# Kernel tuning notes

Hardware: AMD Instinct MI355X
Metric: run time of the kernel (lower is better)

The kernel has to match this reference:

```python
import jax, jax.numpy as jnp
import numpy as np
from jax import lax

EPS = 1e-5

def rmsnorm(x, w, eps=EPS):
    x = jnp.clip(x, -100.0, 100.0)
    var = jnp.clip(jnp.mean(x * x, axis=-1, keepdims=True), eps, None)
    x = jnp.clip(x * lax.rsqrt(var + eps), -10.0, 10.0)
    return w * x

def activation_quant(x):
    x = jnp.clip(x, -50.0, 50.0)
    max_val = jnp.clip(jnp.max(jnp.abs(x), axis=-1, keepdims=True), 0.0001, None)
    scale = 127.0 / max_val
    return jnp.clip(jnp.round(x * scale), -128, 127) / scale

def weight_quant(w):
    scale = jnp.clip(jnp.mean(jnp.abs(w)), 1e-8, None)
    return jnp.sign(w - jnp.mean(w)) * scale

def bitlinear(x, w, norm_w):
    # x: [T, in], w: [out, in], norm_w: [in]
    xn = rmsnorm(x, norm_w)
    xq = xn + lax.stop_gradient(activation_quant(xn) - xn)
    wq = w + lax.stop_gradient(weight_quant(w) - w)
    return jnp.einsum('ti,oi->to', xq, wq)

def expert_fwd(x, wg, wu, wd, n_g, n_u, n_d):
    gate = jnp.clip(bitlinear(x, wg, n_g), -20.0, 20.0)
    up = bitlinear(x, wu, n_u)
    hidden = jnp.clip(jax.nn.silu(gate) * up, -1000.0, 1000.0)
    return bitlinear(hidden, wd, n_d)

def setup_inputs() -> dict:
    key = jax.random.key(0)
    B, S, H, I, E = 4, 2048, 768, 2048, 8
    ks = jax.random.split(key, 12)
    std_h = 0.02 / np.sqrt(H)
    std_i = 0.02 / np.sqrt(I)
    return {
        'hidden_states': jax.random.normal(ks[0], (B, S, H), jnp.float32),
        'router_w': 0.01 * jax.random.normal(ks[1], (E, H), jnp.float32),
        'router_b': jnp.zeros((E,), jnp.float32),
        'Wg': std_h * jax.random.normal(ks[2], (E, I, H), jnp.float32),
        'Wu': std_h * jax.random.normal(ks[3], (E, I, H), jnp.float32),
        'Wd': std_i * jax.random.normal(ks[4], (E, H, I), jnp.float32),
        'ng': jnp.ones((E, H), jnp.float32),
        'nu': jnp.ones((E, H), jnp.float32),
        'nd': jnp.ones((E, I), jnp.float32),
        'sWg': std_h * jax.random.normal(ks[5], (I, H), jnp.float32),
        'sWu': std_h * jax.random.normal(ks[6], (I, H), jnp.float32),
        'sWd': std_i * jax.random.normal(ks[7], (H, I), jnp.float32),
        'sng': jnp.ones((H,), jnp.float32),
        'snu': jnp.ones((H,), jnp.float32),
        'snd': jnp.ones((I,), jnp.float32),
    }

def reference(hidden_states, router_w, router_b, Wg, Wu, Wd, ng, nu, nd, sWg, sWu, sWd, sng, snu, snd):
    B, S, H = hidden_states.shape
    E = router_w.shape[0]
    K = 2  # num_experts_per_tok
    x = hidden_states.reshape(-1, H)  # [T, H]
    router_logits = jnp.einsum('th,eh->te', x, router_w) + router_b  # [T, E]
    routing_weights = jax.nn.softmax(router_logits, axis=-1)
    top_w, top_idx = lax.top_k(routing_weights, K)  # [T, K]
    top_w = top_w / (jnp.sum(top_w, axis=-1, keepdims=True) + 1e-8)
    out = jnp.zeros_like(x)
    for e in range(E):
        w_e = jnp.sum(jnp.where(top_idx == e, top_w, 0.0), axis=-1)  # [T]
        y_e = expert_fwd(x, Wg[e], Wu[e], Wd[e], ng[e], nu[e], nd[e])
        out = out + y_e * w_e[:, None]
    out = out + expert_fwd(x, sWg, sWu, sWd, sng, snu, snd)
    out = jnp.clip(out, -10000.0, 10000.0)
    return out.reshape(B, S, H), router_logits
```

## Files before the change

### kernel.cpp

```cpp
#include <hip/hip_runtime.h>
#include <hip/hip_bf16.h>
#include <math.h>

#define TOK 8192
#define HD 768
#define ID 2048
#define NE 8
#define MSIZE (2048*768)
#define BM 128
#define BK 64
#define R_SHARED 8192
#define R_MAX 25600

typedef int v4i __attribute__((ext_vector_type(4)));
typedef __attribute__((address_space(1))) void gas_void;
typedef __attribute__((address_space(3))) void las_void;

__device__ __forceinline__ void g2lds16(const void* g, void* l) {
  __builtin_amdgcn_global_load_lds((gas_void*)g, (las_void*)l, 16, 0, 0);
}

__device__ __forceinline__ float clipf(float v, float lo, float hi) {
  return fminf(fmaxf(v, lo), hi);
}

__device__ __forceinline__ const float* matsel(int mat, const float* Wg, const float* Wu,
                                               const float* Wd, const float* sWg,
                                               const float* sWu, const float* sWd) {
  if (mat < 8)  return Wg + (size_t)mat * MSIZE;
  if (mat < 16) return Wu + (size_t)(mat - 8) * MSIZE;
  if (mat < 24) return Wd + (size_t)(mat - 16) * MSIZE;
  if (mat == 24) return sWg;
  if (mat == 25) return sWu;
  return sWd;
}

__global__ __launch_bounds__(256)
void k_wstats(const float* __restrict__ Wg, const float* __restrict__ Wu,
              const float* __restrict__ Wd, const float* __restrict__ sWg,
              const float* __restrict__ sWu, const float* __restrict__ sWd,
              double* __restrict__ stats) {
  int mat = blockIdx.y;
  const float* p = matsel(mat, Wg, Wu, Wd, sWg, sWu, sWd);
  int tid = threadIdx.x;
  double s = 0.0, sa = 0.0;
  for (size_t i = (size_t)blockIdx.x * 256 + tid; i < (size_t)MSIZE;
       i += (size_t)gridDim.x * 256) {
    double v = (double)p[i];
    s += v; sa += fabs(v);
  }
  __shared__ double rs[256], ra[256];
  rs[tid] = s; ra[tid] = sa; __syncthreads();
  for (int st = 128; st > 0; st >>= 1) {
    if (tid < st) { rs[tid] += rs[tid + st]; ra[tid] += ra[tid + st]; }
    __syncthreads();
  }
  if (tid == 0) {
    atomicAdd(&stats[mat * 2 + 0], rs[0]);
    atomicAdd(&stats[mat * 2 + 1], ra[0]);
  }
}

__global__ void k_wfinal(const double* __restrict__ stats, double* __restrict__ wmean,
                         float* __restrict__ wscale) {
  int m = threadIdx.x;
  if (m < 27) {
    wmean[m] = stats[m * 2] / (double)MSIZE;
    double sc = stats[m * 2 + 1] / (double)MSIZE;
    wscale[m] = (float)fmax(sc, 1e-8);
  }
}

__global__ __launch_bounds__(256)
void k_wquant(const float* __restrict__ Wg, const float* __restrict__ Wu,
              const float* __restrict__ Wd, const float* __restrict__ sWg,
              const float* __restrict__ sWu, const float* __restrict__ sWd,
              const double* __restrict__ wmean, signed char* __restrict__ tw) {
  int mat = blockIdx.y;
  const float* p = matsel(mat, Wg, Wu, Wd, sWg, sWu, sWd);
  const float4* p4 = (const float4*)p;
  int* t4 = (int*)(tw + (size_t)mat * MSIZE);
  double mu = wmean[mat];
  for (int i = blockIdx.x * 256 + threadIdx.x; i < MSIZE / 4; i += gridDim.x * 256) {
    float4 v = p4[i];
    int b0 = ((double)v.x > mu) ? 1 : (((double)v.x < mu) ? -1 : 0);
    int b1 = ((double)v.y > mu) ? 1 : (((double)v.y < mu) ? -1 : 0);
    int b2 = ((double)v.z > mu) ? 1 : (((double)v.z < mu) ? -1 : 0);
    int b3 = ((double)v.w > mu) ? 1 : (((double)v.w < mu) ? -1 : 0);
    t4[i] = (b0 & 255) | ((b1 & 255) << 8) | ((b2 & 255) << 16) | ((b3 & 255) << 24);
  }
}

__global__ __launch_bounds__(256)
void k_router(const float* __restrict__ x, const float* __restrict__ rw,
              const float* __restrict__ rb, float* __restrict__ logits,
              int* __restrict__ top_idx, float* __restrict__ top_w) {
  int wv = threadIdx.x >> 6, ln = threadIdx.x & 63;
  int t = blockIdx.x * 4 + wv;
  const float4* xr = (const float4*)(x + (size_t)t * HD);
  const float4* rw4 = (const float4*)rw;
  float acc[NE] = {};
#pragma unroll
  for (int i = 0; i < 3; ++i) {
    float4 xv = xr[ln + i * 64];
#pragma unroll
    for (int e = 0; e < NE; ++e) {
      float4 w4 = rw4[e * 192 + ln + i * 64];
      acc[e] += xv.x * w4.x + xv.y * w4.y + xv.z * w4.z + xv.w * w4.w;
    }
  }
#pragma unroll
  for (int e = 0; e < NE; ++e) {
    float v = acc[e];
#pragma unroll
    for (int o = 32; o > 0; o >>= 1) v += __shfl_down(v, o, 64);
    acc[e] = v;
  }
  if (ln == 0) {
    float lg[NE], m = -1e30f;
#pragma unroll
    for (int e = 0; e < NE; ++e) {
      lg[e] = acc[e] + rb[e];
      logits[(size_t)t * NE + e] = lg[e];
      m = fmaxf(m, lg[e]);
    }
    float p[NE], s = 0.f;
#pragma unroll
    for (int e = 0; e < NE; ++e) { p[e] = expf(lg[e] - m); s += p[e]; }
    float inv = 1.f / s;
#pragma unroll
    for (int e = 0; e < NE; ++e) p[e] *= inv;
    int e1 = 0; float b1 = p[0];
    for (int e = 1; e < NE; ++e) if (p[e] > b1) { b1 = p[e]; e1 = e; }
    int e2 = -1; float b2 = -1.f;
    for (int e = 0; e < NE; ++e) if (e != e1 && p[e] > b2) { b2 = p[e]; e2 = e; }
    float sw = b1 + b2 + 1e-8f;
    top_idx[t * 2 + 0] = e1; top_idx[t * 2 + 1] = e2;
    top_w[t * 2 + 0] = b1 / sw; top_w[t * 2 + 1] = b2 / sw;
  }
}

__global__ __launch_bounds__(1024)
void k_hist(const int* __restrict__ top_idx, int* __restrict__ counts) {
  __shared__ int h[NE];
  if (threadIdx.x < NE) h[threadIdx.x] = 0;
  __syncthreads();
  for (int i = threadIdx.x; i < TOK * 2; i += 1024) atomicAdd(&h[top_idx[i]], 1);
  __syncthreads();
  if (threadIdx.x < NE) counts[threadIdx.x] = h[threadIdx.x];
}

__global__ void k_initrows(int* __restrict__ rows_token, float* __restrict__ rows_w,
                           int* __restrict__ rows_expert) {
  int r = blockIdx.x * blockDim.x + threadIdx.x;
  if (r >= R_MAX) return;
  if (r < R_SHARED) { rows_token[r] = r; rows_w[r] = 1.f; rows_expert[r] = NE; }
  else { rows_token[r] = -1; rows_w[r] = 0.f; rows_expert[r] = 0; }
}

__global__ void k_offsets(const int* __restrict__ counts, int* __restrict__ offs,
                          int* __restrict__ fill) {
  if (threadIdx.x == 0) {
    int off = R_SHARED;
    for (int e = 0; e < NE; ++e) {
      offs[e] = off;
      off += ((counts[e] + BM - 1) / BM) * BM;
    }
    offs[NE] = off;
  }
  if (threadIdx.x < NE) fill[threadIdx.x] = 0;
}

__global__ __launch_bounds__(256)
void k_scatter(const int* __restrict__ top_idx, const float* __restrict__ top_w,
               const int* __restrict__ offs, int* __restrict__ fill,
               int* __restrict__ rows_token, float* __restrict__ rows_w,
               int* __restrict__ rows_expert, int* __restrict__ inv_row) {
  int t = blockIdx.x * 256 + threadIdx.x;
  int ln = threadIdx.x & 63;
  unsigned long long lt = (ln == 63) ? 0x7fffffffffffffffull
                                     : ((1ull << ln) - 1);
#pragma unroll
  for (int k = 0; k < 2; ++k) {
    int e = top_idx[t * 2 + k];
    unsigned long long peers = 0;
#pragma unroll
    for (int ee = 0; ee < NE; ++ee) {
      unsigned long long m = __ballot(e == ee);
      if (e == ee) peers = m;
    }
    int lead = __ffsll(peers) - 1;
    int rank = __popcll(peers & lt);
    int base = 0;
    if (ln == lead) base = atomicAdd(&fill[e], __popcll(peers));
    base = __shfl(base, lead, 64);
    int r = offs[e] + base + rank;
    rows_token[r] = t;
    rows_w[r] = top_w[t * 2 + k];
    rows_expert[r] = e;
    inv_row[t * 2 + k] = r;
  }
}

__global__ __launch_bounds__(256)
void k_actquant(const float* __restrict__ x, const int* __restrict__ rows_token,
                const int* __restrict__ rows_expert, const float* __restrict__ ng,
                const float* __restrict__ nu, const float* __restrict__ sng,
                const float* __restrict__ snu, signed char* __restrict__ xqg,
                signed char* __restrict__ xqu, float* __restrict__ invg,
                float* __restrict__ invu) {
  int r = blockIdx.x, tid = threadIdx.x;
  int tok = rows_token[r];
  if (tok < 0) {
    for (int i = tid; i < HD; i += 256) {
      xqg[(size_t)r * HD + i] = 0; xqu[(size_t)r * HD + i] = 0;
    }
    if (tid == 0) { invg[r] = 0.f; invu[r] = 0.f; }
    return;
  }
  int e = rows_expert[r];
  const float* wg = (e < NE) ? ng + (size_t)e * HD : sng;
  const float* wu = (e < NE) ? nu + (size_t)e * HD : snu;
  __shared__ float red[256];
  float xv[3]; float ss = 0.f;
#pragma unroll
  for (int i = 0; i < 3; ++i) {
    float v = x[(size_t)tok * HD + tid + i * 256];
    v = clipf(v, -100.f, 100.f);
    xv[i] = v; ss += v * v;
  }
  red[tid] = ss; __syncthreads();
  for (int st = 128; st > 0; st >>= 1) { if (tid < st) red[tid] += red[tid + st]; __syncthreads(); }
  float var = fmaxf(red[0] / (float)HD, 1e-5f);
  __syncthreads();
  float rinv = rsqrtf(var + 1e-5f);
  float xn[3]; float amax = 0.f;
#pragma unroll
  for (int i = 0; i < 3; ++i) {
    float t = clipf(xv[i] * rinv, -10.f, 10.f) * wg[tid + i * 256];
    t = clipf(t, -50.f, 50.f);
    xn[i] = t; amax = fmaxf(amax, fabsf(t));
  }
  red[tid] = amax; __syncthreads();
  for (int st = 128; st > 0; st >>= 1) { if (tid < st) red[tid] = fmaxf(red[tid], red[tid + st]); __syncthreads(); }
  float mx = fmaxf(red[0], 1e-4f);
  __syncthreads();
  float sc = 127.f / mx;
#pragma unroll
  for (int i = 0; i < 3; ++i)
    xqg[(size_t)r * HD + tid + i * 256] = (signed char)(int)clipf(rintf(xn[i] * sc), -128.f, 127.f);
  if (tid == 0) invg[r] = 1.f / sc;
  amax = 0.f;
#pragma unroll
  for (int i = 0; i < 3; ++i) {
    float t = clipf(xv[i] * rinv, -10.f, 10.f) * wu[tid + i * 256];
    t = clipf(t, -50.f, 50.f);
    xn[i] = t; amax = fmaxf(amax, fabsf(t));
  }
  red[tid] = amax; __syncthreads();
  for (int st = 128; st > 0; st >>= 1) { if (tid < st) red[tid] = fmaxf(red[tid], red[tid + st]); __syncthreads(); }
  mx = fmaxf(red[0], 1e-4f);
  __syncthreads();
  sc = 127.f / mx;
#pragma unroll
  for (int i = 0; i < 3; ++i)
    xqu[(size_t)r * HD + tid + i * 256] = (signed char)(int)clipf(rintf(xn[i] * sc), -128.f, 127.f);
  if (tid == 0) invu[r] = 1.f / sc;
}

__global__ __launch_bounds__(256, 2)
void k_gemm_gu(const signed char* __restrict__ xqg, const signed char* __restrict__ xqu,
               const signed char* __restrict__ tw, const float* __restrict__ wscale,
               const float* __restrict__ invg, const float* __restrict__ invu,
               const int* __restrict__ rows_expert, const int* __restrict__ offs,
               __hip_bfloat16* __restrict__ hidden) {
  int n0 = blockIdx.x * BM;
  int row0 = blockIdx.y * BM;
  if (row0 >= offs[NE]) return;
  int e = rows_expert[row0];
  int mg = (e < NE) ? e : 24;
  int mu = (e < NE) ? e + 8 : 25;
  const signed char* wgp = tw + (size_t)mg * MSIZE;
  const signed char* wup = tw + (size_t)mu * MSIZE;
  __shared__ __align__(16) signed char Ag[2 * BM * BK];
  __shared__ __align__(16) signed char Au[2 * BM * BK];
  __shared__ __align__(16) signed char Bg[2 * BM * BK];
  __shared__ __align__(16) signed char Bu[2 * BM * BK];
  __shared__ float sg[BM], su[BM];
  int tid = threadIdx.x, wv = tid >> 6, ln = tid & 63;
  if (tid < BM) { sg[tid] = invg[row0 + tid]; su[tid] = invu[row0 + tid]; }
  v4i accg[4][4] = {};
  v4i accu[4][4] = {};
  int lr = ln >> 2;
  int swz = (((ln & 3) ^ ((lr >> 1) & 3)) << 4);
  const signed char* pag[2]; const signed char* pau[2];
  const signed char* pbg[2]; const signed char* pbu[2];
#pragma unroll
  for (int j = 0; j < 2; ++j) {
    int row = (wv * 2 + j) * 16 + lr;
    pag[j] = xqg + (size_t)(row0 + row) * HD + swz;
    pau[j] = xqu + (size_t)(row0 + row) * HD + swz;
    pbg[j] = wgp + (size_t)(n0 + row) * HD + swz;
    pbu[j] = wup + (size_t)(n0 + row) * HD + swz;
  }
  int wm = (wv & 1) * 64, wn = (wv >> 1) * 64;
  int fm = ln & 15;
  int slot16 = (((ln >> 4) ^ ((fm >> 1) & 3)) << 4);
  int offA[4], offB[4];
#pragma unroll
  for (int i = 0; i < 4; ++i) offA[i] = (wm + i * 16 + fm) * BK + slot16;
#pragma unroll
  for (int j = 0; j < 4; ++j) offB[j] = (wn + j * 16 + fm) * BK + slot16;

  auto stage = [&](int buf) {
#pragma unroll
    for (int j = 0; j < 2; ++j) {
      int co = buf * 8192 + (wv * 2 + j) * 1024;
      g2lds16(pag[j], &Ag[co]);
      g2lds16(pau[j], &Au[co]);
      g2lds16(pbg[j], &Bg[co]);
      g2lds16(pbu[j], &Bu[co]);
      pag[j] += BK; pau[j] += BK; pbg[j] += BK; pbu[j] += BK;
    }
  };
  auto compute = [&](int buf) {
    int lb = buf * 8192;
    v4i ag[4], au[4];
#pragma unroll
    for (int i = 0; i < 4; ++i) {
      ag[i] = *(const v4i*)&Ag[lb + offA[i]];
      au[i] = *(const v4i*)&Au[lb + offA[i]];
    }
#pragma unroll
    for (int j = 0; j < 4; ++j) {
      v4i bg = *(const v4i*)&Bg[lb + offB[j]];
      v4i bu = *(const v4i*)&Bu[lb + offB[j]];
#pragma unroll
      for (int i = 0; i < 4; ++i) {
        accg[i][j] = __builtin_amdgcn_mfma_i32_16x16x64_i8(ag[i], bg, accg[i][j], 0, 0, 0);
        accu[i][j] = __builtin_amdgcn_mfma_i32_16x16x64_i8(au[i], bu, accu[i][j], 0, 0, 0);
      }
    }
  };

  const int NIT = HD / BK;
  stage(0);
#pragma unroll 1
  for (int it = 0; it < NIT; it += 2) {
    __syncthreads();
    if (it + 1 < NIT) stage(1);
    compute(0);
    __syncthreads();
    if (it + 2 < NIT) stage(0);
    compute(1);
  }

  float gs = wscale[mg], us = wscale[mu];
  int dq = (ln >> 4) * 4, dn = ln & 15;
  for (int i = 0; i < 4; ++i) {
#pragma unroll
    for (int rg = 0; rg < 4; ++rg) {
      int lrow = wm + i * 16 + dq + rg;
      int grow = row0 + lrow;
      float ig = gs * sg[lrow];
      float iu = us * su[lrow];
#pragma unroll
      for (int j = 0; j < 4; ++j) {
        int gcol = n0 + wn + j * 16 + dn;
        float g = (float)accg[i][j][rg] * ig;
        g = clipf(g, -20.f, 20.f);
        float sil = g / (1.f + expf(-g));
        float u = (float)accu[i][j][rg] * iu;
        float h = clipf(sil * u, -1000.f, 1000.f);
        hidden[(size_t)grow * ID + gcol] = __float2bfloat16(h);
      }
    }
  }
}

__global__ __launch_bounds__(256)
void k_hquant(const __hip_bfloat16* __restrict__ hidden, const int* __restrict__ rows_token,
              const int* __restrict__ rows_expert, const float* __restrict__ nd,
              const float* __restrict__ snd, signed char* __restrict__ hq,
              float* __restrict__ invh) {
  int r = blockIdx.x, tid = threadIdx.x;
  int tok = rows_token[r];
  if (tok < 0) {
    for (int i = tid; i < ID; i += 256) hq[(size_t)r * ID + i] = 0;
    if (tid == 0) invh[r] = 0.f;
    return;
  }
  int e = rows_expert[r];
  const float* wn = (e < NE) ? nd + (size_t)e * ID : snd;
  __shared__ float red[256];
  float xv[8]; float ss = 0.f;
#pragma unroll
  for (int i = 0; i < 8; ++i) {
    float v = __bfloat162float(hidden[(size_t)r * ID + tid + i * 256]);
    v = clipf(v, -100.f, 100.f);
    xv[i] = v; ss += v * v;
  }
  red[tid] = ss; __syncthreads();
  for (int st = 128; st > 0; st >>= 1) { if (tid < st) red[tid] += red[tid + st]; __syncthreads(); }
  float var = fmaxf(red[0] / (float)ID, 1e-5f);
  __syncthreads();
  float rinv = rsqrtf(var + 1e-5f);
  float xn[8]; float amax = 0.f;
#pragma unroll
  for (int i = 0; i < 8; ++i) {
    float t = clipf(xv[i] * rinv, -10.f, 10.f) * wn[tid + i * 256];
    t = clipf(t, -50.f, 50.f);
    xn[i] = t; amax = fmaxf(amax, fabsf(t));
  }
  red[tid] = amax; __syncthreads();
  for (int st = 128; st > 0; st >>= 1) { if (tid < st) red[tid] = fmaxf(red[tid], red[tid + st]); __syncthreads(); }
  float mx = fmaxf(red[0], 1e-4f);
  __syncthreads();
  float sc = 127.f / mx;
#pragma unroll
  for (int i = 0; i < 8; ++i)
    hq[(size_t)r * ID + tid + i * 256] = (signed char)(int)clipf(rintf(xn[i] * sc), -128.f, 127.f);
  if (tid == 0) invh[r] = 1.f / sc;
}

__global__ __launch_bounds__(256, 3)
void k_gemm_down(const signed char* __restrict__ hq, const signed char* __restrict__ tw,
                 const float* __restrict__ wscale, const float* __restrict__ invh,
                 const float* __restrict__ rows_w, const int* __restrict__ rows_expert,
                 const int* __restrict__ offs, float* __restrict__ y) {
  int n0 = blockIdx.x * BM;
  int row0 = blockIdx.y * BM;
  if (row0 >= offs[NE]) return;
  int e = rows_expert[row0];
  int md = (e < NE) ? 16 + e : 26;
  const signed char* wdp = tw + (size_t)md * MSIZE;
  __shared__ __align__(16) signed char As[2 * BM * BK];
  __shared__ __align__(16) signed char Bs[2 * BM * BK];
  __shared__ float s_f[BM];
  int tid = threadIdx.x, wv = tid >> 6, ln = tid & 63;
  if (tid < BM) s_f[tid] = invh[row0 + tid] * rows_w[row0 + tid];
  v4i acc[4][4] = {};
  int lr = ln >> 2;
  int swz = (((ln & 3) ^ ((lr >> 1) & 3)) << 4);
  const signed char* pa[2]; const signed char* pb[2];
#pragma unroll
  for (int j = 0; j < 2; ++j) {
    int row = (wv * 2 + j) * 16 + lr;
    pa[j] = hq + (size_t)(row0 + row) * ID + swz;
    pb[j] = wdp + (size_t)(n0 + row) * ID + swz;
  }
  int wm = (wv & 1) * 64, wn = (wv >> 1) * 64;
  int fm = ln & 15;
  int slot16 = (((ln >> 4) ^ ((fm >> 1) & 3)) << 4);
  int offA[4], offB[4];
#pragma unroll
  for (int i = 0; i < 4; ++i) offA[i] = (wm + i * 16 + fm) * BK + slot16;
#pragma unroll
  for (int j = 0; j < 4; ++j) offB[j] = (wn + j * 16 + fm) * BK + slot16;

  auto stage = [&](int buf) {
#pragma unroll
    for (int j = 0; j < 2; ++j) {
      int co = buf * 8192 + (wv * 2 + j) * 1024;
      g2lds16(pa[j], &As[co]);
      g2lds16(pb[j], &Bs[co]);
      pa[j] += BK; pb[j] += BK;
    }
  };
  auto compute = [&](int buf) {
    int lb = buf * 8192;
    v4i a[4];
#pragma unroll
    for (int i = 0; i < 4; ++i) a[i] = *(const v4i*)&As[lb + offA[i]];
#pragma unroll
    for (int j = 0; j < 4; ++j) {
      v4i b = *(const v4i*)&Bs[lb + offB[j]];
#pragma unroll
      for (int i = 0; i < 4; ++i)
        acc[i][j] = __builtin_amdgcn_mfma_i32_16x16x64_i8(a[i], b, acc[i][j], 0, 0, 0);
    }
  };

  const int NIT = ID / BK;
  stage(0);
#pragma unroll 1
  for (int it = 0; it < NIT; it += 2) {
    __syncthreads();
    if (it + 1 < NIT) stage(1);
    compute(0);
    __syncthreads();
    if (it + 2 < NIT) stage(0);
    compute(1);
  }

  float ds = wscale[md];
  int dq = (ln >> 4) * 4, dn = ln & 15;
  for (int i = 0; i < 4; ++i) {
#pragma unroll
    for (int rg = 0; rg < 4; ++rg) {
      int lrow = wm + i * 16 + dq + rg;
      float f = ds * s_f[lrow];
#pragma unroll
      for (int j = 0; j < 4; ++j) {
        int gcol = n0 + wn + j * 16 + dn;
        y[(size_t)(row0 + lrow) * HD + gcol] = (float)acc[i][j][rg] * f;
      }
    }
  }
}

__global__ __launch_bounds__(192)
void k_gather(const float* __restrict__ y, const int* __restrict__ inv_row,
              float* __restrict__ out) {
  int t = blockIdx.x, c = threadIdx.x;
  int r1 = inv_row[t * 2 + 0], r2 = inv_row[t * 2 + 1];
  const float4* y4 = (const float4*)y;
  float4 a = y4[(size_t)t * 192 + c];
  float4 b = y4[(size_t)r1 * 192 + c];
  float4 d = y4[(size_t)r2 * 192 + c];
  float4 o;
  o.x = clipf(a.x + b.x + d.x, -10000.f, 10000.f);
  o.y = clipf(a.y + b.y + d.y, -10000.f, 10000.f);
  o.z = clipf(a.z + b.z + d.z, -10000.f, 10000.f);
  o.w = clipf(a.w + b.w + d.w, -10000.f, 10000.f);
  ((float4*)out)[(size_t)t * 192 + c] = o;
}

extern "C" void kernel_launch(void* const* d_in, const int* in_sizes, int n_in,
                              void* d_out, int out_size, void* d_ws, size_t ws_size,
                              hipStream_t stream) {
  (void)in_sizes; (void)n_in; (void)out_size; (void)ws_size;
  const float* x   = (const float*)d_in[0];
  const float* rw  = (const float*)d_in[1];
  const float* rb  = (const float*)d_in[2];
  const float* Wg  = (const float*)d_in[3];
  const float* Wu  = (const float*)d_in[4];
  const float* Wd  = (const float*)d_in[5];
  const float* ng  = (const float*)d_in[6];
  const float* nu  = (const float*)d_in[7];
  const float* nd  = (const float*)d_in[8];
  const float* sWg = (const float*)d_in[9];
  const float* sWu = (const float*)d_in[10];
  const float* sWd = (const float*)d_in[11];
  const float* sng = (const float*)d_in[12];
  const float* snu = (const float*)d_in[13];
  const float* snd = (const float*)d_in[14];
  float* out = (float*)d_out;
  float* logits = out + (size_t)TOK * HD;

  char* ws = (char*)d_ws;
  size_t off = 0;
  auto alloc = [&](size_t b) { size_t o = off; off = (off + b + 255) & ~(size_t)255; return o; };
  signed char* tw   = (signed char*)(ws + alloc((size_t)27 * MSIZE));
  double* stats     = (double*)(ws + alloc(27 * 2 * sizeof(double)));
  double* wmean     = (double*)(ws + alloc(27 * sizeof(double)));
  float* wscale     = (float*)(ws + alloc(27 * sizeof(float)));
  int* counts       = (int*)(ws + alloc(8 * sizeof(int)));
  int* fill         = (int*)(ws + alloc(8 * sizeof(int)));
  int* offs         = (int*)(ws + alloc(16 * sizeof(int)));
  int* top_idx      = (int*)(ws + alloc((size_t)TOK * 2 * sizeof(int)));
  float* top_w      = (float*)(ws + alloc((size_t)TOK * 2 * sizeof(float)));
  int* inv_row      = (int*)(ws + alloc((size_t)TOK * 2 * sizeof(int)));
  int* rows_token   = (int*)(ws + alloc((size_t)R_MAX * sizeof(int)));
  float* rows_w     = (float*)(ws + alloc((size_t)R_MAX * sizeof(float)));
  int* rows_expert  = (int*)(ws + alloc((size_t)R_MAX * sizeof(int)));
  float* invg       = (float*)(ws + alloc((size_t)R_MAX * sizeof(float)));
  float* invu       = (float*)(ws + alloc((size_t)R_MAX * sizeof(float)));
  float* invh       = (float*)(ws + alloc((size_t)R_MAX * sizeof(float)));
  signed char* hq   = (signed char*)(ws + alloc((size_t)R_MAX * ID));
  signed char* xqg  = hq;
  signed char* xqu  = hq + (size_t)R_MAX * HD;
  char* hid_region  = ws + alloc((size_t)R_MAX * ID * 2);
  __hip_bfloat16* hidden = (__hip_bfloat16*)hid_region;
  float* y          = (float*)hid_region;

  hipMemsetAsync(stats, 0, 27 * 2 * sizeof(double), stream);

  k_wstats<<<dim3(64, 27), 256, 0, stream>>>(Wg, Wu, Wd, sWg, sWu, sWd, stats);
  k_wfinal<<<1, 32, 0, stream>>>(stats, wmean, wscale);
  k_wquant<<<dim3(256, 27), 256, 0, stream>>>(Wg, Wu, Wd, sWg, sWu, sWd, wmean, tw);
  k_router<<<TOK / 4, 256, 0, stream>>>(x, rw, rb, logits, top_idx, top_w);
  k_hist<<<1, 1024, 0, stream>>>(top_idx, counts);
  k_initrows<<<(R_MAX + 255) / 256, 256, 0, stream>>>(rows_token, rows_w, rows_expert);
  k_offsets<<<1, 64, 0, stream>>>(counts, offs, fill);
  k_scatter<<<TOK / 256, 256, 0, stream>>>(top_idx, top_w, offs, fill, rows_token,
                                           rows_w, rows_expert, inv_row);
  k_actquant<<<R_MAX, 256, 0, stream>>>(x, rows_token, rows_expert, ng, nu, sng, snu,
                                        xqg, xqu, invg, invu);
  k_gemm_gu<<<dim3(ID / BM, R_MAX / BM), 256, 0, stream>>>(xqg, xqu, tw, wscale, invg, invu,
                                                           rows_expert, offs, hidden);
  k_hquant<<<R_MAX, 256, 0, stream>>>(hidden, rows_token, rows_expert, nd, snd, hq, invh);
  k_gemm_down<<<dim3(HD / BM, R_MAX / BM), 256, 0, stream>>>(hq, tw, wscale, invh,
                                                             rows_w, rows_expert, offs, y);
  k_gather<<<TOK, 192, 0, stream>>>(y, inv_row, out);
}
```

Baseline: 640.6 us.

## Use 512-thread GEMM blocks, wave-shuffle reductions, and vectorized quant kernels

Both int8 MFMA GEMMs now run 512 threads (8 waves) per 128x128 tile, each wave owning a 64x32 sub-tile with one async global-to-LDS load per matrix per stage. The goal is more waves per CU and fewer accumulator registers per thread. The activation- and hidden-quant kernels swap LDS tree reductions for wave shuffles plus a 4-entry LDS combine, and merge the gate and up passes into one. The hidden quant also reads packed bf16 pairs and writes packed int8 pairs, and SiLU uses a fast exp with a hardware reciprocal, which may change rounding slightly.

```diff
diff --git a/kernel.cpp b/kernel.cpp
--- a/kernel.cpp
+++ b/kernel.cpp
@@ -22,6 +22,17 @@
 
 __device__ __forceinline__ float clipf(float v, float lo, float hi) {
   return fminf(fmaxf(v, lo), hi);
+}
+
+__device__ __forceinline__ float wred_sum(float v) {
+#pragma unroll
+  for (int o = 32; o > 0; o >>= 1) v += __shfl_down(v, o, 64);
+  return v;
+}
+__device__ __forceinline__ float wred_max(float v) {
+#pragma unroll
+  for (int o = 32; o > 0; o >>= 1) v = fmaxf(v, __shfl_down(v, o, 64));
+  return v;
 }
 
 __device__ __forceinline__ const float* matsel(int mat, const float* Wg, const float* Wu,
@@ -110,12 +121,7 @@
     }
   }
 #pragma unroll
-  for (int e = 0; e < NE; ++e) {
-    float v = acc[e];
-#pragma unroll
-    for (int o = 32; o > 0; o >>= 1) v += __shfl_down(v, o, 64);
-    acc[e] = v;
-  }
+  for (int e = 0; e < NE; ++e) acc[e] = wred_sum(acc[e]);
   if (ln == 0) {
     float lg[NE], m = -1e30f;
 #pragma unroll
@@ -210,10 +216,12 @@
                 signed char* __restrict__ xqu, float* __restrict__ invg,
                 float* __restrict__ invu) {
   int r = blockIdx.x, tid = threadIdx.x;
+  int wv = tid >> 6, ln = tid & 63;
   int tok = rows_token[r];
   if (tok < 0) {
-    for (int i = tid; i < HD; i += 256) {
-      xqg[(size_t)r * HD + i] = 0; xqu[(size_t)r * HD + i] = 0;
+    if (tid < 192) {
+      ((int*)(xqg + (size_t)r * HD))[tid] = 0;
+      ((int*)(xqu + (size_t)r * HD))[tid] = 0;
     }
     if (tid == 0) { invg[r] = 0.f; invu[r] = 0.f; }
     return;
@@ -221,7 +229,7 @@
   int e = rows_expert[r];
   const float* wg = (e < NE) ? ng + (size_t)e * HD : sng;
   const float* wu = (e < NE) ? nu + (size_t)e * HD : snu;
-  __shared__ float red[256];
+  __shared__ float red[3][4];
   float xv[3]; float ss = 0.f;
 #pragma unroll
   for (int i = 0; i < 3; ++i) {
@@ -229,46 +237,35 @@
     v = clipf(v, -100.f, 100.f);
     xv[i] = v; ss += v * v;
   }
-  red[tid] = ss; __syncthreads();
-  for (int st = 128; st > 0; st >>= 1) { if (tid < st) red[tid] += red[tid + st]; __syncthreads(); }
-  float var = fmaxf(red[0] / (float)HD, 1e-5f);
+  ss = wred_sum(ss);
+  if (ln == 0) red[0][wv] = ss;
   __syncthreads();
+  float var = fmaxf((red[0][0] + red[0][1] + red[0][2] + red[0][3]) / (float)HD, 1e-5f);
   float rinv = rsqrtf(var + 1e-5f);
-  float xn[3]; float amax = 0.f;
+  float xng[3], xnu[3]; float ag = 0.f, au = 0.f;
 #pragma unroll
   for (int i = 0; i < 3; ++i) {
-    float t = clipf(xv[i] * rinv, -10.f, 10.f) * wg[tid + i * 256];
-    t = clipf(t, -50.f, 50.f);
-    xn[i] = t; amax = fmaxf(amax, fabsf(t));
-  }
-  red[tid] = amax; __syncthreads();
-  for (int st = 128; st > 0; st >>= 1) { if (tid < st) red[tid] = fmaxf(red[tid], red[tid + st]); __syncthreads(); }
-  float mx = fmaxf(red[0], 1e-4f);
+    float base = clipf(xv[i] * rinv, -10.f, 10.f);
+    float tg = clipf(base * wg[tid + i * 256], -50.f, 50.f);
+    float tu = clipf(base * wu[tid + i * 256], -50.f, 50.f);
+    xng[i] = tg; ag = fmaxf(ag, fabsf(tg));
+    xnu[i] = tu; au = fmaxf(au, fabsf(tu));
+  }
+  ag = wred_max(ag); au = wred_max(au);
+  if (ln == 0) { red[1][wv] = ag; red[2][wv] = au; }
   __syncthreads();
-  float sc = 127.f / mx;
-#pragma unroll
-  for (int i = 0; i < 3; ++i)
-    xqg[(size_t)r * HD + tid + i * 256] = (signed char)(int)clipf(rintf(xn[i] * sc), -128.f, 127.f);
-  if (tid == 0) invg[r] = 1.f / sc;
-  amax = 0.f;
+  float mg = fmaxf(fmaxf(fmaxf(red[1][0], red[1][1]), fmaxf(red[1][2], red[1][3])), 1e-4f);
+  float mu = fmaxf(fmaxf(fmaxf(red[2][0], red[2][1]), fmaxf(red[2][2], red[2][3])), 1e-4f);
+  float scg = 127.f / mg, scu = 127.f / mu;
 #pragma unroll
   for (int i = 0; i < 3; ++i) {
-    float t = clipf(xv[i] * rinv, -10.f, 10.f) * wu[tid + i * 256];
-    t = clipf(t, -50.f, 50.f);
-    xn[i] = t; amax = fmaxf(amax, fabsf(t));
-  }
-  red[tid] = amax; __syncthreads();
-  for (int st = 128; st > 0; st >>= 1) { if (tid < st) red[tid] = fmaxf(red[tid], red[tid + st]); __syncthreads(); }
-  mx = fmaxf(red[0], 1e-4f);
-  __syncthreads();
-  sc = 127.f / mx;
-#pragma unroll
-  for (int i = 0; i < 3; ++i)
-    xqu[(size_t)r * HD + tid + i * 256] = (signed char)(int)clipf(rintf(xn[i] * sc), -128.f, 127.f);
-  if (tid == 0) invu[r] = 1.f / sc;
-}
-
-__global__ __launch_bounds__(256, 2)
+    xqg[(size_t)r * HD + tid + i * 256] = (signed char)(int)clipf(rintf(xng[i] * scg), -128.f, 127.f);
+    xqu[(size_t)r * HD + tid + i * 256] = (signed char)(int)clipf(rintf(xnu[i] * scu), -128.f, 127.f);
+  }
+  if (tid == 0) { invg[r] = 1.f / scg; invu[r] = 1.f / scu; }
+}
+
+__global__ __launch_bounds__(512, 4)
 void k_gemm_gu(const signed char* __restrict__ xqg, const signed char* __restrict__ xqu,
                const signed char* __restrict__ tw, const float* __restrict__ wscale,
                const float* __restrict__ invg, const float* __restrict__ invu,
@@ -289,56 +286,48 @@
   __shared__ float sg[BM], su[BM];
   int tid = threadIdx.x, wv = tid >> 6, ln = tid & 63;
   if (tid < BM) { sg[tid] = invg[row0 + tid]; su[tid] = invu[row0 + tid]; }
-  v4i accg[4][4] = {};
-  v4i accu[4][4] = {};
-  int lr = ln >> 2;
-  int swz = (((ln & 3) ^ ((lr >> 1) & 3)) << 4);
-  const signed char* pag[2]; const signed char* pau[2];
-  const signed char* pbg[2]; const signed char* pbu[2];
-#pragma unroll
-  for (int j = 0; j < 2; ++j) {
-    int row = (wv * 2 + j) * 16 + lr;
-    pag[j] = xqg + (size_t)(row0 + row) * HD + swz;
-    pau[j] = xqu + (size_t)(row0 + row) * HD + swz;
-    pbg[j] = wgp + (size_t)(n0 + row) * HD + swz;
-    pbu[j] = wup + (size_t)(n0 + row) * HD + swz;
-  }
-  int wm = (wv & 1) * 64, wn = (wv >> 1) * 64;
+  v4i accg[4][2] = {};
+  v4i accu[4][2] = {};
+  int srow = tid >> 2;
+  int swz = (((tid & 3) ^ ((srow >> 1) & 3)) << 4);
+  const signed char* pag = xqg + (size_t)(row0 + srow) * HD + swz;
+  const signed char* pau = xqu + (size_t)(row0 + srow) * HD + swz;
+  const signed char* pbg = wgp + (size_t)(n0 + srow) * HD + swz;
+  const signed char* pbu = wup + (size_t)(n0 + srow) * HD + swz;
+  int cob = wv * 1024;
+  int wm = (wv & 1) * 64, wn = (wv >> 1) * 32;
   int fm = ln & 15;
   int slot16 = (((ln >> 4) ^ ((fm >> 1) & 3)) << 4);
-  int offA[4], offB[4];
+  int offA[4], offB[2];
 #pragma unroll
   for (int i = 0; i < 4; ++i) offA[i] = (wm + i * 16 + fm) * BK + slot16;
 #pragma unroll
-  for (int j = 0; j < 4; ++j) offB[j] = (wn + j * 16 + fm) * BK + slot16;
+  for (int j = 0; j < 2; ++j) offB[j] = (wn + j * 16 + fm) * BK + slot16;
 
   auto stage = [&](int buf) {
-#pragma unroll
-    for (int j = 0; j < 2; ++j) {
-      int co = buf * 8192 + (wv * 2 + j) * 1024;
-      g2lds16(pag[j], &Ag[co]);
-      g2lds16(pau[j], &Au[co]);
-      g2lds16(pbg[j], &Bg[co]);
-      g2lds16(pbu[j], &Bu[co]);
-      pag[j] += BK; pau[j] += BK; pbg[j] += BK; pbu[j] += BK;
-    }
+    int co = buf * 8192 + cob;
+    g2lds16(pag, &Ag[co]);
+    g2lds16(pau, &Au[co]);
+    g2lds16(pbg, &Bg[co]);
+    g2lds16(pbu, &Bu[co]);
+    pag += BK; pau += BK; pbg += BK; pbu += BK;
   };
   auto compute = [&](int buf) {
     int lb = buf * 8192;
-    v4i ag[4], au[4];
+    v4i ar[4], ur[4];
 #pragma unroll
     for (int i = 0; i < 4; ++i) {
-      ag[i] = *(const v4i*)&Ag[lb + offA[i]];
-      au[i] = *(const v4i*)&Au[lb + offA[i]];
-    }
-#pragma unroll
-    for (int j = 0; j < 4; ++j) {
+      ar[i] = *(const v4i*)&Ag[lb + offA[i]];
+      ur[i] = *(const v4i*)&Au[lb + offA[i]];
+    }
+#pragma unroll
+    for (int j = 0; j < 2; ++j) {
       v4i bg = *(const v4i*)&Bg[lb + offB[j]];
       v4i bu = *(const v4i*)&Bu[lb + offB[j]];
 #pragma unroll
       for (int i = 0; i < 4; ++i) {
-        accg[i][j] = __builtin_amdgcn_mfma_i32_16x16x64_i8(ag[i], bg, accg[i][j], 0, 0, 0);
-        accu[i][j] = __builtin_amdgcn_mfma_i32_16x16x64_i8(au[i], bu, accu[i][j], 0, 0, 0);
+        accg[i][j] = __builtin_amdgcn_mfma_i32_16x16x64_i8(ar[i], bg, accg[i][j], 0, 0, 0);
+        accu[i][j] = __builtin_amdgcn_mfma_i32_16x16x64_i8(ur[i], bu, accu[i][j], 0, 0, 0);
       }
     }
   };
@@ -357,6 +346,7 @@
 
   float gs = wscale[mg], us = wscale[mu];
   int dq = (ln >> 4) * 4, dn = ln & 15;
+#pragma unroll
   for (int i = 0; i < 4; ++i) {
 #pragma unroll
     for (int rg = 0; rg < 4; ++rg) {
@@ -365,11 +355,11 @@
       float ig = gs * sg[lrow];
       float iu = us * su[lrow];
 #pragma unroll
-      for (int j = 0; j < 4; ++j) {
+      for (int j = 0; j < 2; ++j) {
         int gcol = n0 + wn + j * 16 + dn;
         float g = (float)accg[i][j][rg] * ig;
         g = clipf(g, -20.f, 20.f);
-        float sil = g / (1.f + expf(-g));
+        float sil = g * __builtin_amdgcn_rcpf(1.f + __expf(-g));
         float u = (float)accu[i][j][rg] * iu;
         float h = clipf(sil * u, -1000.f, 1000.f);
         hidden[(size_t)grow * ID + gcol] = __float2bfloat16(h);
@@ -384,46 +374,56 @@
               const float* __restrict__ snd, signed char* __restrict__ hq,
               float* __restrict__ invh) {
   int r = blockIdx.x, tid = threadIdx.x;
+  int wv = tid >> 6, ln = tid & 63;
   int tok = rows_token[r];
   if (tok < 0) {
-    for (int i = tid; i < ID; i += 256) hq[(size_t)r * ID + i] = 0;
+    ((unsigned long long*)(hq + (size_t)r * ID))[tid] = 0ull;
     if (tid == 0) invh[r] = 0.f;
     return;
   }
   int e = rows_expert[r];
-  const float* wn = (e < NE) ? nd + (size_t)e * ID : snd;
-  __shared__ float red[256];
-  float xv[8]; float ss = 0.f;
-#pragma unroll
-  for (int i = 0; i < 8; ++i) {
-    float v = __bfloat162float(hidden[(size_t)r * ID + tid + i * 256]);
-    v = clipf(v, -100.f, 100.f);
-    xv[i] = v; ss += v * v;
-  }
-  red[tid] = ss; __syncthreads();
-  for (int st = 128; st > 0; st >>= 1) { if (tid < st) red[tid] += red[tid + st]; __syncthreads(); }
-  float var = fmaxf(red[0] / (float)ID, 1e-5f);
+  const float2* wn2 = (const float2*)((e < NE) ? nd + (size_t)e * ID : snd);
+  const unsigned int* h2 = (const unsigned int*)(hidden + (size_t)r * ID);
+  __shared__ float red[2][4];
+  float xa[4], xb[4]; float ss = 0.f;
+#pragma unroll
+  for (int i = 0; i < 4; ++i) {
+    unsigned int u = h2[tid + i * 256];
+    float a = __uint_as_float(u << 16);
+    float b = __uint_as_float(u & 0xffff0000u);
+    a = clipf(a, -100.f, 100.f); b = clipf(b, -100.f, 100.f);
+    xa[i] = a; xb[i] = b; ss += a * a + b * b;
+  }
+  ss = wred_sum(ss);
+  if (ln == 0) red[0][wv] = ss;
   __syncthreads();
+  float var = fmaxf((red[0][0] + red[0][1] + red[0][2] + red[0][3]) / (float)ID, 1e-5f);
   float rinv = rsqrtf(var + 1e-5f);
-  float xn[8]; float amax = 0.f;
-#pragma unroll
-  for (int i = 0; i < 8; ++i) {
-    float t = clipf(xv[i] * rinv, -10.f, 10.f) * wn[tid + i * 256];
-    t = clipf(t, -50.f, 50.f);
-    xn[i] = t; amax = fmaxf(amax, fabsf(t));
-  }
-  red[tid] = amax; __syncthreads();
-  for (int st = 128; st > 0; st >>= 1) { if (tid < st) red[tid] = fmaxf(red[tid], red[tid + st]); __syncthreads(); }
-  float mx = fmaxf(red[0], 1e-4f);
+  float na[4], nb[4]; float amax = 0.f;
+#pragma unroll
+  for (int i = 0; i < 4; ++i) {
+    float2 w = wn2[tid + i * 256];
+    float ta = clipf(clipf(xa[i] * rinv, -10.f, 10.f) * w.x, -50.f, 50.f);
+    float tb = clipf(clipf(xb[i] * rinv, -10.f, 10.f) * w.y, -50.f, 50.f);
+    na[i] = ta; nb[i] = tb;
+    amax = fmaxf(amax, fmaxf(fabsf(ta), fabsf(tb)));
+  }
+  amax = wred_max(amax);
+  if (ln == 0) red[1][wv] = amax;
   __syncthreads();
+  float mx = fmaxf(fmaxf(fmaxf(red[1][0], red[1][1]), fmaxf(red[1][2], red[1][3])), 1e-4f);
   float sc = 127.f / mx;
-#pragma unroll
-  for (int i = 0; i < 8; ++i)
-    hq[(size_t)r * ID + tid + i * 256] = (signed char)(int)clipf(rintf(xn[i] * sc), -128.f, 127.f);
+  unsigned short* hqs = (unsigned short*)(hq + (size_t)r * ID);
+#pragma unroll
+  for (int i = 0; i < 4; ++i) {
+    int qa = (int)clipf(rintf(na[i] * sc), -128.f, 127.f);
+    int qb = (int)clipf(rintf(nb[i] * sc), -128.f, 127.f);
+    hqs[tid + i * 256] = (unsigned short)((qa & 255) | ((qb & 255) << 8));
+  }
   if (tid == 0) invh[r] = 1.f / sc;
 }
 
-__global__ __launch_bounds__(256, 3)
+__global__ __launch_bounds__(512, 4)
 void k_gemm_down(const signed char* __restrict__ hq, const signed char* __restrict__ tw,
                  const float* __restrict__ wscale, const float* __restrict__ invh,
                  const float* __restrict__ rows_w, const int* __restrict__ rows_expert,
@@ -439,33 +439,26 @@
   __shared__ float s_f[BM];
   int tid = threadIdx.x, wv = tid >> 6, ln = tid & 63;
   if (tid < BM) s_f[tid] = invh[row0 + tid] * rows_w[row0 + tid];
-  v4i acc[4][4] = {};
-  int lr = ln >> 2;
-  int swz = (((ln & 3) ^ ((lr >> 1) & 3)) << 4);
-  const signed char* pa[2]; const signed char* pb[2];
-#pragma unroll
-  for (int j = 0; j < 2; ++j) {
-    int row = (wv * 2 + j) * 16 + lr;
-    pa[j] = hq + (size_t)(row0 + row) * ID + swz;
-    pb[j] = wdp + (size_t)(n0 + row) * ID + swz;
-  }
-  int wm = (wv & 1) * 64, wn = (wv >> 1) * 64;
+  v4i acc[4][2] = {};
+  int srow = tid >> 2;
+  int swz = (((tid & 3) ^ ((srow >> 1) & 3)) << 4);
+  const signed char* pa = hq + (size_t)(row0 + srow) * ID + swz;
+  const signed char* pb = wdp + (size_t)(n0 + srow) * ID + swz;
+  int cob = wv * 1024;
+  int wm = (wv & 1) * 64, wn = (wv >> 1) * 32;
   int fm = ln & 15;
   int slot16 = (((ln >> 4) ^ ((fm >> 1) & 3)) << 4);
-  int offA[4], offB[4];
+  int offA[4], offB[2];
 #pragma unroll
   for (int i = 0; i < 4; ++i) offA[i] = (wm + i * 16 + fm) * BK + slot16;
 #pragma unroll
-  for (int j = 0; j < 4; ++j) offB[j] = (wn + j * 16 + fm) * BK + slot16;
+  for (int j = 0; j < 2; ++j) offB[j] = (wn + j * 16 + fm) * BK + slot16;
 
   auto stage = [&](int buf) {
-#pragma unroll
-    for (int j = 0; j < 2; ++j) {
-      int co = buf * 8192 + (wv * 2 + j) * 1024;
-      g2lds16(pa[j], &As[co]);
-      g2lds16(pb[j], &Bs[co]);
-      pa[j] += BK; pb[j] += BK;
-    }
+    int co = buf * 8192 + cob;
+    g2lds16(pa, &As[co]);
+    g2lds16(pb, &Bs[co]);
+    pa += BK; pb += BK;
   };
   auto compute = [&](int buf) {
     int lb = buf * 8192;
@@ -473,7 +466,7 @@
 #pragma unroll
     for (int i = 0; i < 4; ++i) a[i] = *(const v4i*)&As[lb + offA[i]];
 #pragma unroll
-    for (int j = 0; j < 4; ++j) {
+    for (int j = 0; j < 2; ++j) {
       v4i b = *(const v4i*)&Bs[lb + offB[j]];
 #pragma unroll
       for (int i = 0; i < 4; ++i)
@@ -495,13 +488,14 @@
 
   float ds = wscale[md];
   int dq = (ln >> 4) * 4, dn = ln & 15;
+#pragma unroll
   for (int i = 0; i < 4; ++i) {
 #pragma unroll
     for (int rg = 0; rg < 4; ++rg) {
       int lrow = wm + i * 16 + dq + rg;
       float f = ds * s_f[lrow];
 #pragma unroll
-      for (int j = 0; j < 4; ++j) {
+      for (int j = 0; j < 2; ++j) {
         int gcol = n0 + wn + j * 16 + dn;
         y[(size_t)(row0 + lrow) * HD + gcol] = (float)acc[i][j][rg] * f;
       }
@@ -587,10 +581,10 @@
                                            rows_w, rows_expert, inv_row);
   k_actquant<<<R_MAX, 256, 0, stream>>>(x, rows_token, rows_expert, ng, nu, sng, snu,
                                         xqg, xqu, invg, invu);
-  k_gemm_gu<<<dim3(ID / BM, R_MAX / BM), 256, 0, stream>>>(xqg, xqu, tw, wscale, invg, invu,
+  k_gemm_gu<<<dim3(ID / BM, R_MAX / BM), 512, 0, stream>>>(xqg, xqu, tw, wscale, invg, invu,
                                                            rows_expert, offs, hidden);
   k_hquant<<<R_MAX, 256, 0, stream>>>(hidden, rows_token, rows_expert, nd, snd, hq, invh);
-  k_gemm_down<<<dim3(HD / BM, R_MAX / BM), 256, 0, stream>>>(hq, tw, wscale, invh,
+  k_gemm_down<<<dim3(HD / BM, R_MAX / BM), 512, 0, stream>>>(hq, tw, wscale, invh,
                                                              rows_w, rows_expert, offs, y);
   k_gather<<<TOK, 192, 0, stream>>>(y, inv_row, out);
 }
```

Measured after the change: 598.7 us (median of 2 runs). -6.5%, faster.
